# Kernel tuning notes

Measured on AMD Instinct MI355X. Metric: run time of the kernel, lower is better.

Reference implementation:

```python
import jax, jax.numpy as jnp
import numpy as np

N, V, D_RAW, D_FEAT, G, NUM_CLASSES = 16, 12, 200704, 1024, 8, 40


def setup_inputs() -> dict:
    key = jax.random.key(0)
    ks = jax.random.split(key, 16)
    s = 0.02
    raw_feats = jax.random.normal(ks[0], (N, V, D_RAW), dtype=jnp.float32)
    final_views = jax.random.normal(ks[1], (N, V, D_FEAT), dtype=jnp.float32)
    rand_view_num = jax.random.randint(ks[2], (N,), 1, V + 1)
    # score FC: Linear(200704,256)+ReLU, Linear(256,1)+ReLU
    W1 = jax.random.normal(ks[3], (D_RAW, 256), dtype=jnp.float32) * s
    b1 = jnp.zeros((256,), jnp.float32)
    W2 = jax.random.normal(ks[4], (256, 1), dtype=jnp.float32) * s
    b2 = jnp.zeros((1,), jnp.float32)
    # classifier head
    Wf1 = jax.random.normal(ks[5], (D_FEAT, 512), dtype=jnp.float32) * s
    bf1 = jnp.zeros((512,), jnp.float32)
    Wf2 = jax.random.normal(ks[6], (512, 256), dtype=jnp.float32) * s
    bf2 = jnp.zeros((256,), jnp.float32)
    Wl = jax.random.normal(ks[7], (256, NUM_CLASSES), dtype=jnp.float32) * s
    bl = jnp.zeros((NUM_CLASSES,), jnp.float32)
    return {"raw_feats": raw_feats, "final_views": final_views,
            "rand_view_num": rand_view_num,
            "W1": W1, "b1": b1, "W2": W2, "b2": b2,
            "Wf1": Wf1, "bf1": bf1, "Wf2": Wf2, "bf2": bf2,
            "Wl": Wl, "bl": bl}


def _gvcnn_head(raw_feats, final_views, mask, W1, b1, W2, b2, Wf1, bf1, Wf2, bf2, Wl, bl):
    # view scores: FC(raw) -> sigmoid(tanh(abs(.)))
    h = jax.nn.relu(jnp.einsum('nvd,dk->nvk', raw_feats, W1) + b1)
    sraw = jax.nn.relu(h @ W2 + b2)[..., 0]                      # [N, V]
    score = jax.nn.sigmoid(jnp.tanh(jnp.abs(sraw)))              # in (0.5, 0.732)
    # bucket by score into G uniform bins on [0,1): bin = floor(score*G)
    bins = jnp.clip(jnp.floor(score * G).astype(jnp.int32), 0, G - 1)
    onehot = jax.nn.one_hot(bins, G, dtype=score.dtype) * mask[..., None]   # [N, V, G]
    counts = onehot.sum(axis=1)                                  # [N, G]
    safe_cnt = jnp.maximum(counts, 1.0)
    # per-bin mean view feature
    bin_sum = jnp.einsum('nvg,nvd->ngd', onehot, final_views)    # [N, G, D]
    bin_mean = bin_sum / safe_cnt[..., None]
    # per-bin weight: mean over bin members of ceil(score * n_bin)
    w = jnp.ceil(score[:, :, None] * counts[:, None, :]) * onehot  # [N, V, G]
    weight = (w.sum(axis=1) / safe_cnt) * (counts > 0)           # [N, G]
    # weighted fusion of non-empty bins
    desc = jnp.einsum('ng,ngd->nd', weight, bin_mean) / weight.sum(axis=1, keepdims=True)
    # classifier (dropout = identity in eval)
    out = jax.nn.relu(desc @ Wf1 + bf1)
    out = jax.nn.relu(out @ Wf2 + bf2)
    return out @ Wl + bl                                         # [N, num_classes]


def reference(raw_feats, final_views, rand_view_num, W1, b1, W2, b2, Wf1, bf1, Wf2, bf2, Wl, bl):
    mask = (jnp.arange(V)[None, :] < rand_view_num[:, None]).astype(raw_feats.dtype)  # [N, V]
    return _gvcnn_head(raw_feats, final_views, mask, W1, b1, W2, b2, Wf1, bf1, Wf2, bf2, Wl, bl)
```

## Files before the change

### kernel.cpp

```cpp
#include <hip/hip_runtime.h>
#include <math.h>

#define NB 16
#define NV 12
#define NROWS 192
#define DRAW 200704
#define KOUT 256
#define DFEAT 1024
#define NG 8
#define NCLS 40

#define NCHUNK 256
#define KC 784

#define ABASE 0
#define BBASE 24576

#define WS_PART 0
#define WS_HR   50331648
#define WS_Z1   50724864

typedef __attribute__((ext_vector_type(8))) short short8;
typedef __attribute__((ext_vector_type(16))) float f32x16;

__device__ __forceinline__ void cvt4(float4 v, uint2& hi, uint2& lo) {
    unsigned b0 = __float_as_uint(v.x), b1 = __float_as_uint(v.y);
    unsigned b2 = __float_as_uint(v.z), b3 = __float_as_uint(v.w);
    hi.x = (b0 >> 16) | (b1 & 0xffff0000u);
    hi.y = (b2 >> 16) | (b3 & 0xffff0000u);
    float r0 = v.x - __uint_as_float(b0 & 0xffff0000u);
    float r1 = v.y - __uint_as_float(b1 & 0xffff0000u);
    float r2 = v.z - __uint_as_float(b2 & 0xffff0000u);
    float r3 = v.w - __uint_as_float(b3 & 0xffff0000u);
    lo.x = (__float_as_uint(r0) >> 16) | (__float_as_uint(r1) & 0xffff0000u);
    lo.y = (__float_as_uint(r2) >> 16) | (__float_as_uint(r3) & 0xffff0000u);
}

#define K1_LOAD(DA, DB, S1)                                                    \
  {                                                                            \
    const int koff = (S1) * 32;                                                \
    _Pragma("unroll") for (int p = 0; p < 3; ++p) {                            \
      bool ok = aact[p] && (akq[p] * 4 + koff < KC);                           \
      DA[p] = ok ? *(const float4*)(aptr[p] + koff)                            \
                 : make_float4(0.f, 0.f, 0.f, 0.f);                            \
    }                                                                          \
    _Pragma("unroll") for (int q = 0; q < 16; ++q) {                           \
      int dd = ks + q + koff;                                                  \
      DB[q] = (dd < KC) ? bptr[(size_t)(koff + q) * KOUT] : 0.f;               \
    }                                                                          \
  }

#define K1_WRITE(CA, CB)                                                       \
  {                                                                            \
    _Pragma("unroll") for (int p = 0; p < 3; ++p) {                            \
      uint2 hi, lo; cvt4(CA[p], hi, lo);                                       \
      *(uint2*)(smem + awoff[p]) = hi;                                         \
      *(uint2*)(smem + awoff[p] + 1024) = lo;                                  \
    }                                                                          \
    _Pragma("unroll") for (int og = 0; og < 2; ++og) {                         \
      uint2 h0, l0, h1, l1;                                                    \
      cvt4(make_float4(CB[og*8+0], CB[og*8+1], CB[og*8+2], CB[og*8+3]), h0, l0); \
      cvt4(make_float4(CB[og*8+4], CB[og*8+5], CB[og*8+6], CB[og*8+7]), h1, l1); \
      uint4 hv; hv.x = h0.x; hv.y = h0.y; hv.z = h1.x; hv.w = h1.y;            \
      uint4 lv; lv.x = l0.x; lv.y = l0.y; lv.z = l1.x; lv.w = l1.y;            \
      *(uint4*)(smem + bwoff[og]) = hv;                                        \
      *(uint4*)(smem + bwoff[og] + 1024) = lv;                                 \
    }                                                                          \
  }

#define K1_MMA()                                                               \
  {                                                                            \
    _Pragma("unroll") for (int kf = 0; kf < 2; ++kf) {                         \
      short8 ah[3], al[3];                                                     \
      _Pragma("unroll") for (int tm = 0; tm < 3; ++tm) {                       \
        int off = ABASE + (wm * 3 + tm) * 4096 + kf * 2048 + (lane << 4);      \
        ah[tm] = *(const short8*)(smem + off);                                 \
        al[tm] = *(const short8*)(smem + off + 1024);                          \
      }                                                                        \
      _Pragma("unroll") for (int tn = 0; tn < 2; ++tn) {                       \
        int off = BBASE + (wn * 2 + tn) * 4096 + kf * 2048 + (lane << 4);      \
        short8 bh = *(const short8*)(smem + off);                              \
        short8 bl = *(const short8*)(smem + off + 1024);                       \
        _Pragma("unroll") for (int tm = 0; tm < 3; ++tm) {                     \
          acc[tm][tn] = __builtin_amdgcn_mfma_f32_32x32x16_bf16(ah[tm], bh, acc[tm][tn], 0, 0, 0); \
          acc[tm][tn] = __builtin_amdgcn_mfma_f32_32x32x16_bf16(ah[tm], bl, acc[tm][tn], 0, 0, 0); \
          acc[tm][tn] = __builtin_amdgcn_mfma_f32_32x32x16_bf16(al[tm], bh, acc[tm][tn], 0, 0, 0); \
        }                                                                      \
      }                                                                        \
    }                                                                          \
  }

#define K1_STEP(CA, CB, NA, NB_, S, DOLOAD)                                    \
  {                                                                            \
    __builtin_amdgcn_sched_barrier(0);                                         \
    __builtin_amdgcn_s_barrier();                                              \
    __builtin_amdgcn_sched_barrier(0);                                         \
    if (DOLOAD) K1_LOAD(NA, NB_, (S) + 1);                                     \
    K1_WRITE(CA, CB);                                                          \
    asm volatile("s_waitcnt lgkmcnt(0)" ::: "memory");                         \
    __builtin_amdgcn_s_barrier();                                              \
    __builtin_amdgcn_sched_barrier(0);                                         \
    K1_MMA();                                                                  \
  }

__global__ __launch_bounds__(512, 2)
void k1_mfma(const float* __restrict__ raw, const float* __restrict__ W1,
             const int* __restrict__ vnum, float* __restrict__ part)
{
    __shared__ __align__(16) char smem[57344];
    __shared__ char act[NROWS];
    const int t = threadIdx.x;
    const int c = blockIdx.x;
    const int d0 = c * KC;
    if (t < NROWS) act[t] = ((t % NV) < vnum[t / NV]) ? 1 : 0;
    __syncthreads();

    int akq[3];
    bool aact[3];
    const float* aptr[3];
    int awoff[3];
#pragma unroll
    for (int p = 0; p < 3; ++p) {
        int idx = p * 512 + t;
        int row = idx >> 3, kq = idx & 7;
        akq[p] = kq;
        aact[p] = act[row] != 0;
        aptr[p] = raw + (size_t)row * DRAW + d0 + kq * 4;
        awoff[p] = ABASE + (row >> 5) * 4096 + (kq >> 2) * 2048
                 + (((row & 31) + ((kq >> 1) & 1) * 32) << 4) + ((kq & 1) << 3);
    }
    const int col = t & 255;
    const int khalf = t >> 8;
    const int ks = khalf * 16;
    const float* bptr = W1 + (size_t)(d0 + ks) * KOUT + col;
    int bwoff[2];
#pragma unroll
    for (int og = 0; og < 2; ++og)
        bwoff[og] = BBASE + ((col >> 5) << 12) + (khalf << 11)
                  + (((col & 31) + og * 32) << 4);

    const int lane = t & 63;
    const int wave = t >> 6;
    const int wm = wave >> 2, wn = wave & 3;

    f32x16 acc[3][2];
#pragma unroll
    for (int i = 0; i < 3; ++i)
#pragma unroll
        for (int j = 0; j < 2; ++j)
#pragma unroll
            for (int r = 0; r < 16; ++r) acc[i][j][r] = 0.f;

    float4 A0[3], A1[3];
    float B0r[16], B1r[16];
    K1_LOAD(A0, B0r, 0);

#pragma unroll 1
    for (int sp = 0; sp < 12; ++sp) {
        K1_STEP(A0, B0r, A1, B1r, 2 * sp, 1);
        K1_STEP(A1, B1r, A0, B0r, 2 * sp + 1, 1);
    }
    K1_STEP(A0, B0r, A1, B1r, 24, 0);

    const int l31 = lane & 31, lh = lane >> 5;
#pragma unroll
    for (int tm = 0; tm < 3; ++tm) {
        int rowb = wm * 96 + tm * 32 + 4 * lh;
#pragma unroll
        for (int tn = 0; tn < 2; ++tn) {
            int colx = wn * 64 + tn * 32 + l31;
            f32x16 a = acc[tm][tn];
#pragma unroll
            for (int r = 0; r < 16; ++r) {
                int grow = rowb + (r & 3) + 8 * (r >> 2);
                part[((size_t)grow * NCHUNK + c) * KOUT + colx] = a[r];
            }
        }
    }
}

__global__ __launch_bounds__(1024)
void k2_half(const float* __restrict__ part, float* __restrict__ hr)
{
    const int row = blockIdx.x >> 1, half = blockIdx.x & 1, t = threadIdx.x;
    const int col = t & 255, cg = t >> 8;
    __shared__ float red[4][KOUT];
    const float* p = part + ((size_t)row * NCHUNK + half * 128 + cg * 32) * KOUT + col;
    float s = 0.f;
#pragma unroll 8
    for (int i = 0; i < 32; ++i) s += p[(size_t)i * KOUT];
    red[cg][col] = s;
    __syncthreads();
    if (t < 256)
        hr[((size_t)row * 2 + half) * KOUT + col] =
            red[0][col] + red[1][col] + red[2][col] + red[3][col];
}

__global__ __launch_bounds__(512)
void kA(const float* __restrict__ hr, const float* __restrict__ b1,
        const float* __restrict__ W2, const float* __restrict__ b2,
        const int* __restrict__ vnum, const float* __restrict__ fv,
        const float* __restrict__ Wf1, const float* __restrict__ bf1,
        float* __restrict__ z1)
{
    const int n = blockIdx.x >> 2;
    const int js = (blockIdx.x & 3) * 128;
    const int t = threadIdx.x;
    __shared__ float red4[4], sc_s[NV], coeffL[NV], wsum[NG], wt[NG], wtotS;
    __shared__ int cnt[NG];
    __shared__ float descL[DFEAT];
    __shared__ float zred[4][128];
    for (int v = 0; v < NV; ++v) {
        if (t < 256) {
            int row = n * NV + v;
            float s = hr[((size_t)row * 2 + 0) * KOUT + t]
                    + hr[((size_t)row * 2 + 1) * KOUT + t];
            float val = fmaxf(s + b1[t], 0.f) * W2[t];
            for (int o = 32; o > 0; o >>= 1) val += __shfl_down(val, o, 64);
            if ((t & 63) == 0) red4[t >> 6] = val;
        }
        __syncthreads();
        if (t == 0) {
            float sm = red4[0] + red4[1] + red4[2] + red4[3];
            float sraw = fmaxf(sm + b2[0], 0.f);
            sc_s[v] = 1.f / (1.f + expf(-tanhf(fabsf(sraw))));
        }
        __syncthreads();
    }
    if (t < NG) { cnt[t] = 0; wsum[t] = 0.f; }
    __syncthreads();
    const int vn = vnum[n];
    const bool act = (t < NV) && (t < vn);
    float sc = 0.f; int b = 0;
    if (act) {
        sc = sc_s[t];
        b = (int)floorf(sc * 8.f); b = b < 0 ? 0 : (b > 7 ? 7 : b);
        atomicAdd(&cnt[b], 1);
    }
    __syncthreads();
    if (act) atomicAdd(&wsum[b], ceilf(sc * (float)cnt[b]));
    __syncthreads();
    if (t < NG) wt[t] = (cnt[t] > 0) ? wsum[t] / (float)cnt[t] : 0.f;
    __syncthreads();
    if (t == 0) { float x = 0.f; for (int g = 0; g < NG; ++g) x += wt[g]; wtotS = x; }
    __syncthreads();
    if (t < NV) coeffL[t] = act ? wt[b] / ((float)cnt[b] * wtotS) : 0.f;
    __syncthreads();
#pragma unroll
    for (int p = 0; p < 2; ++p) {
        int d = t + p * 512;
        float a = 0.f;
#pragma unroll
        for (int v = 0; v < NV; ++v)
            a = fmaf(coeffL[v], fv[((size_t)n * NV + v) * DFEAT + d], a);
        descL[d] = a;
    }
    __syncthreads();
    {
        const int j = t & 127, kq = t >> 7;
        float a = 0.f;
#pragma unroll 8
        for (int dd = 0; dd < 256; ++dd) {
            int d = kq * 256 + dd;
            a = fmaf(descL[d], Wf1[(size_t)d * 512 + js + j], a);
        }
        zred[kq][j] = a;
    }
    __syncthreads();
    if (t < 128) {
        float s = zred[0][t] + zred[1][t] + zred[2][t] + zred[3][t];
        z1[n * 512 + js + t] = fmaxf(s + bf1[js + t], 0.f);
    }
}

__global__ __launch_bounds__(512)
void kB(const float* __restrict__ z1, const float* __restrict__ Wf2,
        const float* __restrict__ bf2, const float* __restrict__ Wl,
        const float* __restrict__ bl, float* __restrict__ out)
{
    const int n = blockIdx.x, t = threadIdx.x;
    __shared__ float z1L[512], z2L[256], outred[8][NCLS];
    z1L[t] = z1[n * 512 + t];
    __syncthreads();
    if (t < 256) {
        float a = 0.f;
#pragma unroll 8
        for (int d = 0; d < 512; ++d)
            a = fmaf(z1L[d], Wf2[(size_t)d * 256 + t], a);
        z2L[t] = fmaxf(a + bf2[t], 0.f);
    }
    __syncthreads();
    if (t < 320) {
        int j = t % NCLS, seg = t / NCLS;
        float a = 0.f;
#pragma unroll
        for (int dd = 0; dd < 32; ++dd) {
            int d = seg * 32 + dd;
            a = fmaf(z2L[d], Wl[d * NCLS + j], a);
        }
        outred[seg][j] = a;
    }
    __syncthreads();
    if (t < NCLS) {
        float a = bl[t];
#pragma unroll
        for (int s8 = 0; s8 < 8; ++s8) a += outred[s8][t];
        out[n * NCLS + t] = a;
    }
}

extern "C" void kernel_launch(void* const* d_in, const int* in_sizes, int n_in,
                              void* d_out, int out_size, void* d_ws, size_t ws_size,
                              hipStream_t stream)
{
    const float* raw  = (const float*)d_in[0];
    const float* fv   = (const float*)d_in[1];
    const int*   vnum = (const int*)d_in[2];
    const float* W1   = (const float*)d_in[3];
    const float* b1   = (const float*)d_in[4];
    const float* W2   = (const float*)d_in[5];
    const float* b2   = (const float*)d_in[6];
    const float* Wf1  = (const float*)d_in[7];
    const float* bf1  = (const float*)d_in[8];
    const float* Wf2  = (const float*)d_in[9];
    const float* bf2  = (const float*)d_in[10];
    const float* Wl   = (const float*)d_in[11];
    const float* bl   = (const float*)d_in[12];
    float* out = (float*)d_out;
    char* ws = (char*)d_ws;
    float* part = (float*)(ws + WS_PART);
    float* hr   = (float*)(ws + WS_HR);
    float* z1   = (float*)(ws + WS_Z1);

    k1_mfma<<<NCHUNK, 512, 0, stream>>>(raw, W1, vnum, part);
    k2_half<<<2 * NROWS, 1024, 0, stream>>>(part, hr);
    kA<<<4 * NB, 512, 0, stream>>>(hr, b1, W2, b2, vnum, fv, Wf1, bf1, z1);
    kB<<<NB, 512, 0, stream>>>(z1, Wf2, bf2, Wl, bl, out);
}
```

Baseline: 148.5 us.

## Stream GEMM tiles via global_load_lds double buffers, convert to bf16 split at read

The first GEMM kernel now copies fp32 tiles of raw features and W1 straight from global memory into double-buffered LDS with global_load_lds, with an XOR swizzle on the A rows. The bf16 hi/lo split moves from the LDS write stage to the MFMA operand read stage. This is meant to drop the register staging pass and one barrier per step, and to overlap the next tile's copy with the current MFMAs. In exchange, LDS use doubles to 112KB, which forces one block per CU, and the split conversion is repeated by every wave that reads the same data. Inactive rows are no longer zero-filled: they read row 0 of raw, and the last K step clamps its indices instead of masking.

```diff
diff --git a/kernel.cpp b/kernel.cpp
--- a/kernel.cpp
+++ b/kernel.cpp
@@ -13,8 +13,10 @@
 #define NCHUNK 256
 #define KC 784
 
-#define ABASE 0
-#define BBASE 24576
+#define ABUF0 0
+#define ABUF1 24576
+#define BBUF0 49152
+#define BBUF1 81920
 
 #define WS_PART 0
 #define WS_HR   50331648
@@ -36,51 +38,55 @@
     lo.y = (__float_as_uint(r2) >> 16) | (__float_as_uint(r3) & 0xffff0000u);
 }
 
-#define K1_LOAD(DA, DB, S1)                                                    \
+__device__ __forceinline__ short8 mk8(uint2 a, uint2 b) {
+    union { unsigned u[4]; short8 s; } x;
+    x.u[0] = a.x; x.u[1] = a.y; x.u[2] = b.x; x.u[3] = b.y;
+    return x.s;
+}
+
+#define K1_DMA(S1, AB, BB)                                                     \
   {                                                                            \
     const int koff = (S1) * 32;                                                \
     _Pragma("unroll") for (int p = 0; p < 3; ++p) {                            \
-      bool ok = aact[p] && (akq[p] * 4 + koff < KC);                           \
-      DA[p] = ok ? *(const float4*)(aptr[p] + koff)                            \
-                 : make_float4(0.f, 0.f, 0.f, 0.f);                            \
+      int fidx = koff + agx[p];                                                \
+      fidx = fidx < (KC - 4) ? fidx : (KC - 4);                                \
+      const float* g = asrc[p] + fidx;                                         \
+      char* l = smem + (AB) + adst[p];                                         \
+      __builtin_amdgcn_global_load_lds(                                        \
+          (const __attribute__((address_space(1))) void*)g,                    \
+          (__attribute__((address_space(3))) void*)l, 16, 0, 0);               \
     }                                                                          \
-    _Pragma("unroll") for (int q = 0; q < 16; ++q) {                           \
-      int dd = ks + q + koff;                                                  \
-      DB[q] = (dd < KC) ? bptr[(size_t)(koff + q) * KOUT] : 0.f;               \
+    _Pragma("unroll") for (int p = 0; p < 4; ++p) {                            \
+      int kg = d0 + koff + (wave << 2) + p;                                    \
+      kg = kg < DRAW ? kg : (DRAW - 1);                                        \
+      const float* g = W1 + (size_t)kg * KOUT + (lane << 2);                   \
+      char* l = smem + (BB) + bdst[p];                                         \
+      __builtin_amdgcn_global_load_lds(                                        \
+          (const __attribute__((address_space(1))) void*)g,                    \
+          (__attribute__((address_space(3))) void*)l, 16, 0, 0);               \
     }                                                                          \
   }
 
-#define K1_WRITE(CA, CB)                                                       \
+#define K1_MMA(AB, BB, KFN)                                                    \
   {                                                                            \
-    _Pragma("unroll") for (int p = 0; p < 3; ++p) {                            \
-      uint2 hi, lo; cvt4(CA[p], hi, lo);                                       \
-      *(uint2*)(smem + awoff[p]) = hi;                                         \
-      *(uint2*)(smem + awoff[p] + 1024) = lo;                                  \
-    }                                                                          \
-    _Pragma("unroll") for (int og = 0; og < 2; ++og) {                         \
-      uint2 h0, l0, h1, l1;                                                    \
-      cvt4(make_float4(CB[og*8+0], CB[og*8+1], CB[og*8+2], CB[og*8+3]), h0, l0); \
-      cvt4(make_float4(CB[og*8+4], CB[og*8+5], CB[og*8+6], CB[og*8+7]), h1, l1); \
-      uint4 hv; hv.x = h0.x; hv.y = h0.y; hv.z = h1.x; hv.w = h1.y;            \
-      uint4 lv; lv.x = l0.x; lv.y = l0.y; lv.z = l1.x; lv.w = l1.y;            \
-      *(uint4*)(smem + bwoff[og]) = hv;                                        \
-      *(uint4*)(smem + bwoff[og] + 1024) = lv;                                 \
-    }                                                                          \
-  }
-
-#define K1_MMA()                                                               \
-  {                                                                            \
-    _Pragma("unroll") for (int kf = 0; kf < 2; ++kf) {                         \
+    _Pragma("unroll") for (int kf = 0; kf < (KFN); ++kf) {                     \
       short8 ah[3], al[3];                                                     \
       _Pragma("unroll") for (int tm = 0; tm < 3; ++tm) {                       \
-        int off = ABASE + (wm * 3 + tm) * 4096 + kf * 2048 + (lane << 4);      \
-        ah[tm] = *(const short8*)(smem + off);                                 \
-        al[tm] = *(const short8*)(smem + off + 1024);                          \
+        int g0 = kf * 4 + lh2;                                                 \
+        float4 a0 = *(const float4*)(smem + (AB) + aoffA[tm] + (((g0 + 0) ^ ax7[tm]) << 4)); \
+        float4 a1 = *(const float4*)(smem + (AB) + aoffA[tm] + (((g0 + 1) ^ ax7[tm]) << 4)); \
+        uint2 h0, l0, h1, l1;                                                  \
+        cvt4(a0, h0, l0); cvt4(a1, h1, l1);                                    \
+        ah[tm] = mk8(h0, h1); al[tm] = mk8(l0, l1);                            \
       }                                                                        \
       _Pragma("unroll") for (int tn = 0; tn < 2; ++tn) {                       \
-        int off = BBASE + (wn * 2 + tn) * 4096 + kf * 2048 + (lane << 4);      \
-        short8 bh = *(const short8*)(smem + off);                              \
-        short8 bl = *(const short8*)(smem + off + 1024);                       \
+        float bq[8];                                                           \
+        _Pragma("unroll") for (int q = 0; q < 8; ++q)                          \
+          bq[q] = *(const float*)(smem + (BB) + ((kf * 16 + lh * 8 + q) << 10) + bcol4[tn]); \
+        uint2 h0, l0, h1, l1;                                                  \
+        cvt4(make_float4(bq[0], bq[1], bq[2], bq[3]), h0, l0);                 \
+        cvt4(make_float4(bq[4], bq[5], bq[6], bq[7]), h1, l1);                 \
+        short8 bh = mk8(h0, h1), bl = mk8(l0, l1);                             \
         _Pragma("unroll") for (int tm = 0; tm < 3; ++tm) {                     \
           acc[tm][tn] = __builtin_amdgcn_mfma_f32_32x32x16_bf16(ah[tm], bh, acc[tm][tn], 0, 0, 0); \
           acc[tm][tn] = __builtin_amdgcn_mfma_f32_32x32x16_bf16(ah[tm], bl, acc[tm][tn], 0, 0, 0); \
@@ -90,58 +96,53 @@
     }                                                                          \
   }
 
-#define K1_STEP(CA, CB, NA, NB_, S, DOLOAD)                                    \
+#define K1_STEP(RA, RB_, WA, WB_, S, DOLOAD, KFN)                              \
   {                                                                            \
+    if (DOLOAD) K1_DMA((S) + 1, WA, WB_);                                      \
+    K1_MMA(RA, RB_, KFN);                                                      \
+    asm volatile("s_waitcnt vmcnt(0)" ::: "memory");                           \
     __builtin_amdgcn_sched_barrier(0);                                         \
     __builtin_amdgcn_s_barrier();                                              \
     __builtin_amdgcn_sched_barrier(0);                                         \
-    if (DOLOAD) K1_LOAD(NA, NB_, (S) + 1);                                     \
-    K1_WRITE(CA, CB);                                                          \
-    asm volatile("s_waitcnt lgkmcnt(0)" ::: "memory");                         \
-    __builtin_amdgcn_s_barrier();                                              \
-    __builtin_amdgcn_sched_barrier(0);                                         \
-    K1_MMA();                                                                  \
   }
 
-__global__ __launch_bounds__(512, 2)
+__global__ __launch_bounds__(512, 1)
 void k1_mfma(const float* __restrict__ raw, const float* __restrict__ W1,
              const int* __restrict__ vnum, float* __restrict__ part)
 {
-    __shared__ __align__(16) char smem[57344];
-    __shared__ char act[NROWS];
+    __shared__ __align__(16) char smem[114688];
     const int t = threadIdx.x;
     const int c = blockIdx.x;
     const int d0 = c * KC;
-    if (t < NROWS) act[t] = ((t % NV) < vnum[t / NV]) ? 1 : 0;
-    __syncthreads();
-
-    int akq[3];
-    bool aact[3];
-    const float* aptr[3];
-    int awoff[3];
-#pragma unroll
-    for (int p = 0; p < 3; ++p) {
-        int idx = p * 512 + t;
-        int row = idx >> 3, kq = idx & 7;
-        akq[p] = kq;
-        aact[p] = act[row] != 0;
-        aptr[p] = raw + (size_t)row * DRAW + d0 + kq * 4;
-        awoff[p] = ABASE + (row >> 5) * 4096 + (kq >> 2) * 2048
-                 + (((row & 31) + ((kq >> 1) & 1) * 32) << 4) + ((kq & 1) << 3);
-    }
-    const int col = t & 255;
-    const int khalf = t >> 8;
-    const int ks = khalf * 16;
-    const float* bptr = W1 + (size_t)(d0 + ks) * KOUT + col;
-    int bwoff[2];
-#pragma unroll
-    for (int og = 0; og < 2; ++og)
-        bwoff[og] = BBASE + ((col >> 5) << 12) + (khalf << 11)
-                  + (((col & 31) + og * 32) << 4);
-
     const int lane = t & 63;
     const int wave = t >> 6;
     const int wm = wave >> 2, wn = wave & 3;
+    const int l31 = lane & 31, lh = lane >> 5;
+    const int lh2 = lh * 2;
+
+    const float* asrc[3];
+    int agx[3], adst[3];
+#pragma unroll
+    for (int p = 0; p < 3; ++p) {
+        int rp = wave * 24 + p * 8 + (lane >> 3);
+        bool actv = (rp % NV) < vnum[rp / NV];
+        asrc[p] = raw + (actv ? (size_t)rp * DRAW : 0) + d0;
+        agx[p] = (((lane & 7) ^ (rp & 7)) << 2);
+        adst[p] = (wave * 24 + p * 8) * 128;
+    }
+    int bdst[4];
+#pragma unroll
+    for (int p = 0; p < 4; ++p) bdst[p] = ((wave << 2) + p) << 10;
+
+    int aoffA[3], ax7[3], bcol4[2];
+#pragma unroll
+    for (int tm = 0; tm < 3; ++tm) {
+        int row = wm * 96 + tm * 32 + l31;
+        aoffA[tm] = row * 128;
+        ax7[tm] = row & 7;
+    }
+#pragma unroll
+    for (int tn = 0; tn < 2; ++tn) bcol4[tn] = (wn * 64 + tn * 32 + l31) << 2;
 
     f32x16 acc[3][2];
 #pragma unroll
@@ -151,18 +152,18 @@
 #pragma unroll
             for (int r = 0; r < 16; ++r) acc[i][j][r] = 0.f;
 
-    float4 A0[3], A1[3];
-    float B0r[16], B1r[16];
-    K1_LOAD(A0, B0r, 0);
+    K1_DMA(0, ABUF0, BBUF0);
+    asm volatile("s_waitcnt vmcnt(0)" ::: "memory");
+    __builtin_amdgcn_s_barrier();
+    __builtin_amdgcn_sched_barrier(0);
 
 #pragma unroll 1
     for (int sp = 0; sp < 12; ++sp) {
-        K1_STEP(A0, B0r, A1, B1r, 2 * sp, 1);
-        K1_STEP(A1, B1r, A0, B0r, 2 * sp + 1, 1);
-    }
-    K1_STEP(A0, B0r, A1, B1r, 24, 0);
-
-    const int l31 = lane & 31, lh = lane >> 5;
+        K1_STEP(ABUF0, BBUF0, ABUF1, BBUF1, 2 * sp, 1, 2);
+        K1_STEP(ABUF1, BBUF1, ABUF0, BBUF0, 2 * sp + 1, 1, 2);
+    }
+    K1_MMA(ABUF0, BBUF0, 1);
+
 #pragma unroll
     for (int tm = 0; tm < 3; ++tm) {
         int rowb = wm * 96 + tm * 32 + 4 * lh;
```

Measured after the change: 170.0 us. +14.5%, slower.
